# Performance work log

Measured on AMD Instinct MI355X. Metric: run time of the kernel, lower is better.

The kernel has to match this reference:

```python
import jax, jax.numpy as jnp
import numpy as np

B, S, D = 4, 2048, 1024  # batch, seq_len, d_emb (even for Givens pairs)


def givens_rotate(r, x):
    """Apply 2x2 Givens block rotations defined by r [D] to x [..., D]."""
    g = r.reshape(-1, 2)
    g = g / jnp.linalg.norm(g, axis=-1, keepdims=True)  # normalize (cos, sin) pairs
    xp = x.reshape(x.shape[:-1] + (x.shape[-1] // 2, 2))
    c, s = g[:, 0], g[:, 1]
    y0 = c * xp[..., 0] - s * xp[..., 1]
    y1 = c * xp[..., 1] + s * xp[..., 0]
    return jnp.stack([y0, y1], axis=-1).reshape(x.shape)


def setup_inputs() -> dict:
    key = jax.random.key(0)
    k1, k2 = jax.random.split(key, 2)
    Q = jax.random.normal(k1, (B, S, D), dtype=jnp.float32)
    # QKV_rotation.weight ~ U(-1, 1) per original init (before the identity overwrite)
    rot_w = jax.random.uniform(k2, (3, D), dtype=jnp.float32, minval=-1.0, maxval=1.0)
    scale = jnp.array([np.sqrt(D)], dtype=jnp.float32)
    bias = jnp.zeros((), dtype=jnp.float32)
    return {"Q": Q, "rot_w": rot_w, "scale": scale, "bias": bias}


def reference(Q, rot_w, scale, bias):
    # Givens-rotation 'projections' for q/k/v
    q = givens_rotate(rot_w[0], Q)
    k = givens_rotate(rot_w[1], Q)
    v = givens_rotate(rot_w[2], Q)
    # prepend zero time coordinate -> points on the Lorentz model ambient space
    zeros = jnp.zeros(Q.shape[:-1] + (1,), Q.dtype)
    q = jnp.concatenate([zeros, q], axis=-1)[:, None]  # [B,1,S,D+1]
    k = jnp.concatenate([zeros, k], axis=-1)[:, None]
    v = jnp.concatenate([zeros, v], axis=-1)[:, None]
    # Lorentz signature (-, +, +, ...)
    sgn = jnp.concatenate([-jnp.ones((1,), Q.dtype), jnp.ones((q.shape[-1] - 1,), Q.dtype)])
    # cinner(q, k): time-negated inner product -> scores [B,1,S,S]
    cin = jnp.einsum('bhqd,bhkd->bhqk', q * sgn, k)
    attn = jax.nn.softmax((2.0 + 2.0 * cin) / scale + bias, axis=-1)
    # Lorentz mid-point: weighted sum normalized by sqrt(|<m,m>_L|)
    ave = jnp.einsum('bhqk,bhkd->bhqd', attn, v)
    inner = jnp.sum(ave * ave * sgn, axis=-1, keepdims=True)
    denom = jnp.sqrt(jnp.clip(jnp.abs(inner), 1e-8, None))
    out = (ave / denom)[:, 0]  # [B,S,D+1]
    return out[..., 1:]  # drop time coordinate -> [B,S,D]
```

## Files before the change

kernel.cpp:

```cpp
#include <hip/hip_runtime.h>

typedef _Float16 h16;
typedef _Float16 half8 __attribute__((ext_vector_type(8)));
typedef _Float16 half4v __attribute__((ext_vector_type(4)));
typedef float floatx4 __attribute__((ext_vector_type(4)));

static constexpr int Bb_ = 4, S_ = 2048, D_ = 1024;

static __device__ __forceinline__ void gl_lds16(const void* g, void* l) {
  __builtin_amdgcn_global_load_lds(
      (const __attribute__((address_space(1))) unsigned int*)g,
      (__attribute__((address_space(3))) unsigned int*)l, 16, 0, 0);
}

__global__ __launch_bounds__(256) void k_prep_t(const float* __restrict__ Q,
                                                const float* __restrict__ rot,
                                                h16* __restrict__ Qh,
                                                h16* __restrict__ Kh,
                                                h16* __restrict__ VhT,
                                                unsigned int* __restrict__ flags) {
  __shared__ __align__(16) h16 tile[64][64];
  int d0 = blockIdx.x * 64, s0 = blockIdx.y * 64, b = blockIdx.z;
  int t = threadIdx.x;
  if (flags && blockIdx.x == 0 && blockIdx.y == 0 && blockIdx.z == 0 && t < 32)
    flags[t] = 0u;
  const float* Qb = Q + ((size_t)b * S_ + s0) * D_ + d0;
  h16* Qhb = Qh + ((size_t)b * S_ + s0) * D_ + d0;
  h16* Khb = Kh + ((size_t)b * S_ + s0) * D_ + d0;
#pragma unroll
  for (int i = 0; i < 4; ++i) {
    int c = t + 256 * i;
    int row = c >> 4;
    int col = (c & 15) * 4;
    float4 q = *(const float4*)&Qb[(size_t)row * D_ + col];
    int dg = (d0 + col) >> 2;
    float4 r0 = ((const float4*)rot)[dg];
    float4 r1 = ((const float4*)rot)[D_ / 4 + dg];
    float4 r2 = ((const float4*)rot)[2 * D_ / 4 + dg];
    float nq0 = r0.x * r0.x + r0.y * r0.y;
    float nk0 = r1.x * r1.x + r1.y * r1.y;
    float iqk0 = rsqrtf(nq0 * nk0);
    float cc0 = (r0.x * r1.x + r0.y * r1.y) * iqk0;
    float ss0 = (r0.x * r1.y - r0.y * r1.x) * iqk0;
    float y0 = cc0 * q.x - ss0 * q.y;
    float y1 = cc0 * q.y + ss0 * q.x;
    float nq1 = r0.z * r0.z + r0.w * r0.w;
    float nk1 = r1.z * r1.z + r1.w * r1.w;
    float iqk1 = rsqrtf(nq1 * nk1);
    float cc1 = (r0.z * r1.z + r0.w * r1.w) * iqk1;
    float ss1 = (r0.z * r1.w - r0.w * r1.z) * iqk1;
    float y2 = cc1 * q.z - ss1 * q.w;
    float y3 = cc1 * q.w + ss1 * q.z;
    float inv0 = rsqrtf(r2.x * r2.x + r2.y * r2.y);
    float cv0 = r2.x * inv0, sv0 = r2.y * inv0;
    float v0 = cv0 * q.x - sv0 * q.y;
    float v1 = cv0 * q.y + sv0 * q.x;
    float inv1 = rsqrtf(r2.z * r2.z + r2.w * r2.w);
    float cv1 = r2.z * inv1, sv1 = r2.w * inv1;
    float v2 = cv1 * q.z - sv1 * q.w;
    float v3 = cv1 * q.w + sv1 * q.z;
    half4v kh = {(h16)y0, (h16)y1, (h16)y2, (h16)y3};
    half4v qh = {(h16)q.x, (h16)q.y, (h16)q.z, (h16)q.w};
    half4v vh = {(h16)v0, (h16)v1, (h16)v2, (h16)v3};
    *(half4v*)&Qhb[(size_t)row * D_ + col] = qh;
    *(half4v*)&Khb[(size_t)row * D_ + col] = kh;
    int pcol = col ^ ((row >> 3) << 3);
    *(half4v*)&tile[row][pcol] = vh;
  }
  __syncthreads();
  h16* dst = VhT + ((size_t)b * D_ + d0) * S_ + s0;
#pragma unroll
  for (int i = 0; i < 2; ++i) {
    int c = t + 256 * i;
    int drow = c >> 3;
    int sc = (c & 7) * 8;
    int xr = sc;
    half8 v;
#pragma unroll
    for (int j = 0; j < 8; ++j) v[j] = tile[sc + j][drow ^ xr];
    *(half8*)&dst[(size_t)drow * S_ + sc] = v;
  }
}

#define G_FENCE asm volatile("" ::: "memory")
#define G_BAR                     \
  do {                            \
    G_FENCE;                      \
    __builtin_amdgcn_s_barrier(); \
    G_FENCE;                      \
  } while (0)

template <int NF, bool OUT16>
__global__ __launch_bounds__(512, 2) void k_gemm8(
    const char* __restrict__ A, int a_pitch, unsigned long long a_batch,
    const char* __restrict__ Bt, int b_pitch, unsigned long long b_batch,
    void* __restrict__ C, int c_pitch, unsigned long long c_batch, int Kdim,
    const float* __restrict__ scale_p, float* __restrict__ pss,
    unsigned int* __restrict__ flags) {
  constexpr int BNR = NF * 64;
  constexpr int JQ = NF / 2;
  __shared__ __align__(16) h16 As[2][2][256 * 32];
  __shared__ __align__(16) h16 Bs[2][2][BNR * 32];
  const int t = threadIdx.x;
  const int lane = t & 63;
  const int w = t >> 6;
  const int wm = (w >> 2) * 128;
  const int wn = (w & 3) * (NF * 16);
  const int id = blockIdx.x + 8 * (blockIdx.y + 8 * blockIdx.z);
  const int L = (id & 7) * 32 + (id >> 3);
  const int tm = L & 7, tn = (L >> 3) & 7, tz = L >> 6;
  const char* Ab = A + (unsigned long long)tz * a_batch +
                   (unsigned long long)(tm * 256) * (unsigned long long)a_pitch;
  const char* Bb = Bt + (unsigned long long)tz * b_batch +
                   (unsigned long long)(tn * BNR) * (unsigned long long)b_pitch;
  const int srow = t >> 2;
  const int scol = ((t & 3) ^ ((t >> 3) & 3)) << 4;
  const int lds_o = t * 16;
  const int mrow = lane & 15, kc = lane >> 4;
  const int koff = (kc ^ ((mrow >> 1) & 3)) << 3;
  const int NT = Kdim >> 6;

#define SG_A(bf, kt, hm)                                                  \
  do {                                                                    \
    const char* sp_ = Ab +                                                \
                      (unsigned long long)(srow + (hm) * 128) * a_pitch + \
                      (kt) * 128 + scol;                                  \
    gl_lds16(sp_, (char*)&As[bf][0][(hm) * 128 * 32] + lds_o);            \
    gl_lds16(sp_ + 64, (char*)&As[bf][1][(hm) * 128 * 32] + lds_o);       \
  } while (0)
#define SG_B(bf, kt, hm)                                                  \
  do {                                                                    \
    const char* sp_ = Bb +                                                \
                      (unsigned long long)(srow + (hm) * 128) * b_pitch + \
                      (kt) * 128 + scol;                                  \
    gl_lds16(sp_, (char*)&Bs[bf][0][(hm) * 128 * 32] + lds_o);            \
    gl_lds16(sp_ + 64, (char*)&Bs[bf][1][(hm) * 128 * 32] + lds_o);       \
  } while (0)

  half8 ar0[4][2], ar1[4][2], br0[JQ][2], br1[JQ][2];
  floatx4 acc[8][NF];
#pragma unroll
  for (int i = 0; i < 8; ++i)
#pragma unroll
    for (int j = 0; j < NF; ++j) acc[i][j] = (floatx4){0.f, 0.f, 0.f, 0.f};

#define LDA_(bf, mh, DST)                                                \
  do {                                                                   \
    _Pragma("unroll") for (int i_ = 0; i_ < 4; ++i_) {                   \
      DST[i_][0] = *(const half8*)&As[bf][0]                             \
                       [(wm + ((mh) * 4 + i_) * 16 + mrow) * 32 + koff]; \
      DST[i_][1] = *(const half8*)&As[bf][1]                             \
                       [(wm + ((mh) * 4 + i_) * 16 + mrow) * 32 + koff]; \
    }                                                                    \
  } while (0)
#define LDB_(bf, nh, DST)                                                \
  do {                                                                   \
    _Pragma("unroll") for (int j_ = 0; j_ < JQ; ++j_) {                  \
      DST[j_][0] = *(const half8*)&Bs[bf][0]                             \
                       [(wn + ((nh)*JQ + j_) * 16 + mrow) * 32 + koff];  \
      DST[j_][1] = *(const half8*)&Bs[bf][1]                             \
                       [(wn + ((nh)*JQ + j_) * 16 + mrow) * 32 + koff];  \
    }                                                                    \
  } while (0)
#define QUAD(mh, nh, AF, BF)                                                 \
  do {                                                                       \
    __builtin_amdgcn_s_setprio(1);                                           \
    _Pragma("unroll") for (int i_ = 0; i_ < 4; ++i_)                         \
        _Pragma("unroll") for (int j_ = 0; j_ < JQ; ++j_) {                  \
      acc[(mh) * 4 + i_][(nh)*JQ + j_] =                                     \
          __builtin_amdgcn_mfma_f32_16x16x32_f16(                            \
              AF[i_][0], BF[j_][0], acc[(mh) * 4 + i_][(nh)*JQ + j_], 0, 0,  \
              0);                                                            \
      acc[(mh) * 4 + i_][(nh)*JQ + j_] =                                     \
          __builtin_amdgcn_mfma_f32_16x16x32_f16(                            \
              AF[i_][1], BF[j_][1], acc[(mh) * 4 + i_][(nh)*JQ + j_], 0, 0,  \
              0);                                                            \
    }                                                                        \
    __builtin_amdgcn_s_setprio(0);                                           \
  } while (0)

  SG_A(0, 0, 0);
  SG_A(0, 0, 1);
  SG_B(0, 0, 0);
  if constexpr (NF == 4) SG_B(0, 0, 1);
  SG_B(1, 1, 0);
  if constexpr (NF == 4) SG_B(1, 1, 1);
  SG_A(1, 1, 0);
  if constexpr (NF == 4)
    asm volatile("s_waitcnt vmcnt(6)" ::: "memory");
  else
    asm volatile("s_waitcnt vmcnt(4)" ::: "memory");
  G_BAR;
  LDA_(0, 0, ar0);
  LDB_(0, 0, br0);

#define TILE_(bf, nb, u)                                   \
  do {                                                     \
    const int k1_ = ((u) + 1 < NT) ? (u) + 1 : NT - 1;     \
    const int k2_ = ((u) + 2 < NT) ? (u) + 2 : NT - 1;     \
                                                   \
    SG_A(nb, k1_, 1);                                      \
    G_BAR;                                                 \
    LDB_(bf, 1, br1);                                      \
    QUAD(0, 0, ar0, br0);                                  \
                                                   \
    G_BAR;                                                 \
    LDA_(bf, 1, ar1);                                      \
    QUAD(0, 1, ar0, br1);                                  \
                                                   \
    SG_B(bf, k2_, 0);                                      \
    G_BAR;                                                 \
    QUAD(1, 0, ar1, br0);                                  \
                                                   \
    if constexpr (NF == 4) SG_B(bf, k2_, 1);               \
    SG_A(bf, k2_, 0);                                      \
    if constexpr (NF == 4)                                 \
      asm volatile("s_waitcnt vmcnt(6)" ::: "memory");     \
    else                                                   \
      asm volatile("s_waitcnt vmcnt(4)" ::: "memory");     \
    G_BAR;                                                 \
    LDA_(nb, 0, ar0);  \
    LDB_(nb, 0, br0);                                      \
    QUAD(1, 1, ar1, br1);                                  \
  } while (0)

  for (int u = 0; u < NT; u += 2) {
    TILE_(0, 1, u);
    TILE_(1, 0, u + 1);
  }
  asm volatile("s_waitcnt vmcnt(0)" ::: "memory");

  const int m0 = tm * 256 + wm;
  const int n0 = tn * BNR + wn;
  const int ccol = lane & 15;
  const int rq = (lane >> 4) * 4;
  if constexpr (OUT16) {
    const float aexp = 2.0f / scale_p[0];
    h16* Cb = (h16*)C + (unsigned long long)tz * c_batch;
#pragma unroll
    for (int i = 0; i < 8; ++i)
#pragma unroll
      for (int j = 0; j < NF; ++j)
#pragma unroll
        for (int r = 0; r < 4; ++r)
          Cb[(unsigned long long)(m0 + i * 16 + rq + r) * c_pitch +
             (n0 + j * 16 + ccol)] = (h16)__expf(acc[i][j][r] * aexp - 8.0f);
  } else {
    float* Cb = (float*)C + (unsigned long long)tz * c_batch;
    if (pss) {
      const int grp = tz * 8 + tm;
      __syncthreads();
      float* wsum = (float*)&As[0][0][0];
      float* finv = wsum + 4 * 256;
      float part[8][4];
#pragma unroll
      for (int i = 0; i < 8; ++i)
#pragma unroll
        for (int r = 0; r < 4; ++r) {
          float s = acc[i][0][r] * acc[i][0][r];
          if constexpr (NF > 1) s += acc[i][1][r] * acc[i][1][r];
#pragma unroll
          for (int m = 1; m < 16; m <<= 1) s += __shfl_xor(s, m);
          part[i][r] = s;
        }
      if ((lane & 15) == 0) {
#pragma unroll
        for (int i = 0; i < 8; ++i)
#pragma unroll
          for (int r = 0; r < 4; ++r)
            wsum[(w & 3) * 256 + wm + i * 16 + rq + r] = part[i][r];
      }
      __syncthreads();
      if (t < 256) {
        float s = wsum[t] + wsum[256 + t] + wsum[512 + t] + wsum[768 + t];
        __hip_atomic_store(&pss[((unsigned)grp * 8 + tn) * 256 + t], s,
                           __ATOMIC_RELAXED, __HIP_MEMORY_SCOPE_AGENT);
      }
      __syncthreads();
      if (t == 0) {
        __hip_atomic_fetch_add(&flags[grp], 1u, __ATOMIC_ACQ_REL,
                               __HIP_MEMORY_SCOPE_AGENT);
        while (__hip_atomic_load(&flags[grp], __ATOMIC_ACQUIRE,
                                 __HIP_MEMORY_SCOPE_AGENT) < 8u)
          __builtin_amdgcn_s_sleep(2);
      }
      __syncthreads();
      if (t < 256) {
        float ss2 = 0.f;
#pragma unroll
        for (int c = 0; c < 8; ++c)
          ss2 += __hip_atomic_load(&pss[((unsigned)grp * 8 + c) * 256 + t],
                                   __ATOMIC_RELAXED, __HIP_MEMORY_SCOPE_AGENT);
        finv[t] = rsqrtf(fmaxf(ss2, 1e-30f));
      }
      __syncthreads();
#pragma unroll
      for (int i = 0; i < 8; ++i) {
#pragma unroll
        for (int r = 0; r < 4; ++r) {
          const float f = finv[wm + i * 16 + rq + r];
#pragma unroll
          for (int j = 0; j < NF; ++j)
            Cb[(unsigned long long)(m0 + i * 16 + rq + r) * c_pitch +
               (n0 + j * 16 + ccol)] = acc[i][j][r] * f;
        }
      }
    } else {
#pragma unroll
      for (int i = 0; i < 8; ++i)
#pragma unroll
        for (int j = 0; j < NF; ++j)
#pragma unroll
          for (int r = 0; r < 4; ++r)
            Cb[(unsigned long long)(m0 + i * 16 + rq + r) * c_pitch +
               (n0 + j * 16 + ccol)] = acc[i][j][r];
    }
  }
#undef TILE_
#undef QUAD
#undef LDB_
#undef LDA_
#undef SG_B
#undef SG_A
}

__global__ __launch_bounds__(256) void k_epilogue(float* __restrict__ O) {
  int wv = threadIdx.x >> 6, ln = threadIdx.x & 63;
  int row = blockIdx.x * 4 + wv;
  float* base = O + (size_t)row * D_;
  float4 u[4];
#pragma unroll
  for (int r = 0; r < 4; ++r) u[r] = ((const float4*)base)[ln + 64 * r];
  float ss = 0.f;
#pragma unroll
  for (int r = 0; r < 4; ++r)
    ss += u[r].x * u[r].x + u[r].y * u[r].y + u[r].z * u[r].z + u[r].w * u[r].w;
#pragma unroll
  for (int off = 32; off; off >>= 1) ss += __shfl_xor(ss, off);
  float f = rsqrtf(fmaxf(ss, 1e-30f));
#pragma unroll
  for (int r = 0; r < 4; ++r) {
    float4 o;
    o.x = u[r].x * f;
    o.y = u[r].y * f;
    o.z = u[r].z * f;
    o.w = u[r].w * f;
    ((float4*)base)[ln + 64 * r] = o;
  }
}

extern "C" void kernel_launch(void* const* d_in, const int* in_sizes, int n_in,
                              void* d_out, int out_size, void* d_ws, size_t ws_size,
                              hipStream_t stream) {
  const float* Q = (const float*)d_in[0];
  const float* rot = (const float*)d_in[1];
  const float* scale = (const float*)d_in[2];
  float* O = (float*)d_out;
  char* ws = (char*)d_ws;
  const size_t MB = 1024ull * 1024ull;
  h16* Qh = (h16*)(ws);
  h16* Kh = (h16*)(ws + 16 * MB);
  h16* VhT = (h16*)(ws + 32 * MB);
  h16* Sl = (h16*)(ws + 48 * MB);
  float* pss = (float*)(ws + 80 * MB);
  unsigned int* flags = (unsigned int*)(ws + 80 * MB + 256 * 1024);
  const bool fused = ws_size >= 80 * MB + 256 * 1024 + 128;
  if (!fused) {
    pss = nullptr;
    flags = nullptr;
  }

  k_prep_t<<<dim3(D_ / 64, S_ / 64, Bb_), 256, 0, stream>>>(Q, rot, Qh, Kh,
                                                            VhT, flags);
  k_gemm8<4, true><<<dim3(8, 8, 4), 512, 0, stream>>>(
      (const char*)Qh, D_ * 2, (unsigned long long)S_ * D_ * 2,
      (const char*)Kh, D_ * 2, (unsigned long long)S_ * D_ * 2,
      (void*)Sl, S_, (unsigned long long)S_ * S_, D_, scale, nullptr, nullptr);
  k_gemm8<2, false><<<dim3(8, 8, 4), 512, 0, stream>>>(
      (const char*)Sl, S_ * 2, (unsigned long long)S_ * S_ * 2,
      (const char*)VhT, S_ * 2, (unsigned long long)D_ * S_ * 2,
      (void*)O, D_, (unsigned long long)S_ * D_, S_, nullptr, pss, flags);
  if (!fused) k_epilogue<<<dim3(Bb_ * S_ / 4), 256, 0, stream>>>(O);
}
```

Before: 178.0 us.

## Co-locate row-group tiles on one XCD and reduce norms via atomic adds

The second GEMM now remaps block IDs so the 8 column tiles sharing a row group land on the same XCD, so the spin-wait on the group flag and the shared row-norm reductions stay within one XCD. Per-tile partial sums are replaced by float atomic adds into a single per-group buffer, which the prep kernel zeroes. The prep kernel also processes 8 elements per thread with half8 stores instead of 4. Atomic float adds make the reduction order nondeterministic, and the zeroing adds a dependency on the prep kernel.

```diff
diff --git a/kernel.cpp b/kernel.cpp
--- a/kernel.cpp
+++ b/kernel.cpp
@@ -13,59 +13,65 @@
       (__attribute__((address_space(3))) unsigned int*)l, 16, 0, 0);
 }
 
-__global__ __launch_bounds__(256) void k_prep_t(const float* __restrict__ Q,
-                                                const float* __restrict__ rot,
-                                                h16* __restrict__ Qh,
-                                                h16* __restrict__ Kh,
-                                                h16* __restrict__ VhT,
-                                                unsigned int* __restrict__ flags) {
+static __device__ __forceinline__ void rot_pair(float q0, float q1, float a0,
+                                                float a1, float b0, float b1,
+                                                float c0, float c1, float& y0,
+                                                float& y1, float& v0,
+                                                float& v1) {
+  float iqk = rsqrtf((a0 * a0 + a1 * a1) * (b0 * b0 + b1 * b1));
+  float cc = (a0 * b0 + a1 * b1) * iqk;
+  float ss = (a0 * b1 - a1 * b0) * iqk;
+  y0 = cc * q0 - ss * q1;
+  y1 = cc * q1 + ss * q0;
+  float iv = rsqrtf(c0 * c0 + c1 * c1);
+  float cv = c0 * iv, sv = c1 * iv;
+  v0 = cv * q0 - sv * q1;
+  v1 = cv * q1 + sv * q0;
+}
+
+__global__ __launch_bounds__(256) void k_prep_t(
+    const float* __restrict__ Q, const float* __restrict__ rot,
+    h16* __restrict__ Qh, h16* __restrict__ Kh, h16* __restrict__ VhT,
+    float* __restrict__ pss, unsigned int* __restrict__ flags) {
   __shared__ __align__(16) h16 tile[64][64];
   int d0 = blockIdx.x * 64, s0 = blockIdx.y * 64, b = blockIdx.z;
   int t = threadIdx.x;
-  if (flags && blockIdx.x == 0 && blockIdx.y == 0 && blockIdx.z == 0 && t < 32)
-    flags[t] = 0u;
+  int bl = blockIdx.x + 16 * (blockIdx.y + 32 * blockIdx.z);
+  if (flags && bl == 0 && t < 32) flags[t] = 0u;
+  if (pss && t < 4) pss[bl * 4 + t] = 0.f;
   const float* Qb = Q + ((size_t)b * S_ + s0) * D_ + d0;
   h16* Qhb = Qh + ((size_t)b * S_ + s0) * D_ + d0;
   h16* Khb = Kh + ((size_t)b * S_ + s0) * D_ + d0;
 #pragma unroll
-  for (int i = 0; i < 4; ++i) {
+  for (int i = 0; i < 2; ++i) {
     int c = t + 256 * i;
-    int row = c >> 4;
-    int col = (c & 15) * 4;
-    float4 q = *(const float4*)&Qb[(size_t)row * D_ + col];
+    int row = c >> 3;
+    int col = (c & 7) * 8;
+    float4 qa = *(const float4*)&Qb[(size_t)row * D_ + col];
+    float4 qb = *(const float4*)&Qb[(size_t)row * D_ + col + 4];
     int dg = (d0 + col) >> 2;
-    float4 r0 = ((const float4*)rot)[dg];
-    float4 r1 = ((const float4*)rot)[D_ / 4 + dg];
-    float4 r2 = ((const float4*)rot)[2 * D_ / 4 + dg];
-    float nq0 = r0.x * r0.x + r0.y * r0.y;
-    float nk0 = r1.x * r1.x + r1.y * r1.y;
-    float iqk0 = rsqrtf(nq0 * nk0);
-    float cc0 = (r0.x * r1.x + r0.y * r1.y) * iqk0;
-    float ss0 = (r0.x * r1.y - r0.y * r1.x) * iqk0;
-    float y0 = cc0 * q.x - ss0 * q.y;
-    float y1 = cc0 * q.y + ss0 * q.x;
-    float nq1 = r0.z * r0.z + r0.w * r0.w;
-    float nk1 = r1.z * r1.z + r1.w * r1.w;
-    float iqk1 = rsqrtf(nq1 * nk1);
-    float cc1 = (r0.z * r1.z + r0.w * r1.w) * iqk1;
-    float ss1 = (r0.z * r1.w - r0.w * r1.z) * iqk1;
-    float y2 = cc1 * q.z - ss1 * q.w;
-    float y3 = cc1 * q.w + ss1 * q.z;
-    float inv0 = rsqrtf(r2.x * r2.x + r2.y * r2.y);
-    float cv0 = r2.x * inv0, sv0 = r2.y * inv0;
-    float v0 = cv0 * q.x - sv0 * q.y;
-    float v1 = cv0 * q.y + sv0 * q.x;
-    float inv1 = rsqrtf(r2.z * r2.z + r2.w * r2.w);
-    float cv1 = r2.z * inv1, sv1 = r2.w * inv1;
-    float v2 = cv1 * q.z - sv1 * q.w;
-    float v3 = cv1 * q.w + sv1 * q.z;
-    half4v kh = {(h16)y0, (h16)y1, (h16)y2, (h16)y3};
-    half4v qh = {(h16)q.x, (h16)q.y, (h16)q.z, (h16)q.w};
-    half4v vh = {(h16)v0, (h16)v1, (h16)v2, (h16)v3};
-    *(half4v*)&Qhb[(size_t)row * D_ + col] = qh;
-    *(half4v*)&Khb[(size_t)row * D_ + col] = kh;
+    float4 r0a = ((const float4*)rot)[dg];
+    float4 r0b = ((const float4*)rot)[dg + 1];
+    float4 r1a = ((const float4*)rot)[D_ / 4 + dg];
+    float4 r1b = ((const float4*)rot)[D_ / 4 + dg + 1];
+    float4 r2a = ((const float4*)rot)[2 * D_ / 4 + dg];
+    float4 r2b = ((const float4*)rot)[2 * D_ / 4 + dg + 1];
+    float y0, y1, y2, y3, y4, y5, y6, y7;
+    float v0, v1, v2, v3, v4, v5, v6, v7;
+    rot_pair(qa.x, qa.y, r0a.x, r0a.y, r1a.x, r1a.y, r2a.x, r2a.y, y0, y1, v0, v1);
+    rot_pair(qa.z, qa.w, r0a.z, r0a.w, r1a.z, r1a.w, r2a.z, r2a.w, y2, y3, v2, v3);
+    rot_pair(qb.x, qb.y, r0b.x, r0b.y, r1b.x, r1b.y, r2b.x, r2b.y, y4, y5, v4, v5);
+    rot_pair(qb.z, qb.w, r0b.z, r0b.w, r1b.z, r1b.w, r2b.z, r2b.w, y6, y7, v6, v7);
+    half8 qh = {(h16)qa.x, (h16)qa.y, (h16)qa.z, (h16)qa.w,
+                (h16)qb.x, (h16)qb.y, (h16)qb.z, (h16)qb.w};
+    half8 kh = {(h16)y0, (h16)y1, (h16)y2, (h16)y3,
+                (h16)y4, (h16)y5, (h16)y6, (h16)y7};
+    half8 vh = {(h16)v0, (h16)v1, (h16)v2, (h16)v3,
+                (h16)v4, (h16)v5, (h16)v6, (h16)v7};
+    *(half8*)&Qhb[(size_t)row * D_ + col] = qh;
+    *(half8*)&Khb[(size_t)row * D_ + col] = kh;
     int pcol = col ^ ((row >> 3) << 3);
-    *(half4v*)&tile[row][pcol] = vh;
+    *(half8*)&tile[row][pcol] = vh;
   }
   __syncthreads();
   h16* dst = VhT + ((size_t)b * D_ + d0) * S_ + s0;
@@ -107,8 +113,20 @@
   const int wm = (w >> 2) * 128;
   const int wn = (w & 3) * (NF * 16);
   const int id = blockIdx.x + 8 * (blockIdx.y + 8 * blockIdx.z);
-  const int L = (id & 7) * 32 + (id >> 3);
-  const int tm = L & 7, tn = (L >> 3) & 7, tz = L >> 6;
+  int tm, tn, tz, grp;
+  if constexpr (OUT16) {
+    const int L = (id & 7) * 32 + (id >> 3);
+    tm = L & 7;
+    tn = (L >> 3) & 7;
+    tz = L >> 6;
+    grp = 0;
+  } else {
+    const int xcd = id & 7, s2 = id >> 3;
+    grp = xcd * 4 + (s2 >> 3);
+    tn = s2 & 7;
+    tz = grp >> 3;
+    tm = grp & 7;
+  }
   const char* Ab = A + (unsigned long long)tz * a_batch +
                    (unsigned long long)(tm * 256) * (unsigned long long)a_pitch;
   const char* Bb = Bt + (unsigned long long)tz * b_batch +
@@ -248,7 +266,6 @@
   } else {
     float* Cb = (float*)C + (unsigned long long)tz * c_batch;
     if (pss) {
-      const int grp = tz * 8 + tm;
       __syncthreads();
       float* wsum = (float*)&As[0][0][0];
       float* finv = wsum + 4 * 256;
@@ -273,8 +290,8 @@
       __syncthreads();
       if (t < 256) {
         float s = wsum[t] + wsum[256 + t] + wsum[512 + t] + wsum[768 + t];
-        __hip_atomic_store(&pss[((unsigned)grp * 8 + tn) * 256 + t], s,
-                           __ATOMIC_RELAXED, __HIP_MEMORY_SCOPE_AGENT);
+        __hip_atomic_fetch_add(&pss[(unsigned)grp * 256 + t], s,
+                               __ATOMIC_RELAXED, __HIP_MEMORY_SCOPE_AGENT);
       }
       __syncthreads();
       if (t == 0) {
@@ -286,11 +303,9 @@
       }
       __syncthreads();
       if (t < 256) {
-        float ss2 = 0.f;
-#pragma unroll
-        for (int c = 0; c < 8; ++c)
-          ss2 += __hip_atomic_load(&pss[((unsigned)grp * 8 + c) * 256 + t],
-                                   __ATOMIC_RELAXED, __HIP_MEMORY_SCOPE_AGENT);
+        float ss2 = __hip_atomic_load(&pss[(unsigned)grp * 256 + t],
+                                      __ATOMIC_RELAXED,
+                                      __HIP_MEMORY_SCOPE_AGENT);
         finv[t] = rsqrtf(fmaxf(ss2, 1e-30f));
       }
       __syncthreads();
@@ -363,15 +378,15 @@
   h16* VhT = (h16*)(ws + 32 * MB);
   h16* Sl = (h16*)(ws + 48 * MB);
   float* pss = (float*)(ws + 80 * MB);
-  unsigned int* flags = (unsigned int*)(ws + 80 * MB + 256 * 1024);
-  const bool fused = ws_size >= 80 * MB + 256 * 1024 + 128;
+  unsigned int* flags = (unsigned int*)(ws + 80 * MB + 32 * 1024);
+  const bool fused = ws_size >= 80 * MB + 32 * 1024 + 128;
   if (!fused) {
     pss = nullptr;
     flags = nullptr;
   }
 
   k_prep_t<<<dim3(D_ / 64, S_ / 64, Bb_), 256, 0, stream>>>(Q, rot, Qh, Kh,
-                                                            VhT, flags);
+                                                            VhT, pss, flags);
   k_gemm8<4, true><<<dim3(8, 8, 4), 512, 0, stream>>>(
       (const char*)Qh, D_ * 2, (unsigned long long)S_ * D_ * 2,
       (const char*)Kh, D_ * 2, (unsigned long long)S_ * D_ * 2,
```

Result: faster. 174.3 us (-2.0%).
